# Kernel tuning notes

Measured on AMD Instinct MI355X. Metric: run time of the kernel, lower is better.

The kernel has to match this reference:

```python
import jax, jax.numpy as jnp
import numpy as np

B, N, C_IN = 8, 8192, 64
M, K, RADIUS = 1024, 64, 0.2
MLP = [64, 64, 128]


def _fps(pts, m):
    """Iterative farthest point sampling. pts: [N,3] -> [m] int32 indices."""
    n = pts.shape[0]

    def step(carry, _):
        dists, last = carry
        d = jnp.sum((pts - pts[last]) ** 2, axis=-1)          # [N]
        dists = jnp.minimum(dists, d)
        nxt = jnp.argmax(dists).astype(jnp.int32)
        return (dists, nxt), nxt

    init = (jnp.full((n,), 1e10, pts.dtype), jnp.int32(0))
    _, idx = jax.lax.scan(step, init, None, length=m - 1)
    return jnp.concatenate([jnp.zeros((1,), jnp.int32), idx])


def _ball_query(new_xyz, xyz, radius, k):
    """new_xyz: [B,3,M], xyz: [B,3,N] -> [B,M,K] neighbor indices.
    First k points within radius (in index order); padded with first hit."""
    d2 = (jnp.sum(new_xyz ** 2, 1)[:, :, None] + jnp.sum(xyz ** 2, 1)[:, None, :]
          - 2.0 * jnp.einsum('bcm,bcn->bmn', new_xyz, xyz))   # [B,M,N]
    mask = d2 < radius * radius
    # stable argsort of ~mask puts indices of in-radius points first, in order
    order = jnp.argsort(jnp.where(mask, 0, 1).astype(jnp.int32), axis=-1)[..., :k]
    count = jnp.sum(mask, axis=-1)                             # [B,M]
    valid = jnp.arange(k)[None, None, :] < count[..., None]
    return jnp.where(valid, order, order[..., :1])


def _group(x, idx):
    """x: [B,C,N], idx: [B,...] -> [B,C,...] gathered along N."""
    return jax.vmap(lambda a, i: a[:, i])(x, idx)


def _forward(xyz, feature, params):
    # FPS centroid indices (torch runs under no_grad -> stop_gradient)
    pts = jax.lax.stop_gradient(jnp.transpose(xyz, (0, 2, 1)))  # [B,N,3]
    cidx = jax.vmap(lambda p: _fps(p, M))(pts)                  # [B,M]
    new_xyz = _group(xyz, cidx)                                 # [B,3,M]
    nidx = _ball_query(jax.lax.stop_gradient(new_xyz),
                       jax.lax.stop_gradient(xyz), RADIUS, K)   # [B,M,K]
    gxyz = _group(xyz, nidx) - new_xyz[..., None]               # [B,3,M,K]
    x = jnp.concatenate([gxyz, _group(feature, nidx)], axis=1)  # [B,3+C,M,K]
    # SharedMLP: 1x1 conv2d + BN (folded to per-channel scale/bias) + ReLU
    for w, s, b in params:
        x = jax.nn.relu(jnp.einsum('oi,bimk->bomk', w, x)
                        * s[:, None, None] + b[:, None, None])
    return new_xyz, jnp.max(x, axis=3)                          # [B,3,M], [B,128,M]


def setup_inputs() -> dict:
    key = jax.random.key(0)
    ks = jax.random.split(key, 5)
    inp = {
        'xyz': jax.random.normal(ks[0], (B, 3, N), jnp.float32),
        'feature': jax.random.normal(ks[1], (B, C_IN, N), jnp.float32),
    }
    prev = C_IN + 3  # use_xyz=True
    for li, co in enumerate(MLP):
        inp[f'w{li}'] = jax.random.normal(ks[2 + li], (co, prev), jnp.float32) / np.sqrt(prev).astype(np.float32)
        inp[f's{li}'] = jnp.ones((co,), jnp.float32)
        inp[f'b{li}'] = jnp.zeros((co,), jnp.float32)
        prev = co
    return inp


def reference(xyz, feature, w0, s0, b0, w1, s1, b1, w2, s2, b2):
    return _forward(xyz, feature, ((w0, s0, b0), (w1, s1, b1), (w2, s2, b2)))
```

## Files before the change

### kernel.cpp

```cpp
#include <hip/hip_runtime.h>


#define B_ 8
#define N_ 8192
#define M_ 1024
#define K_ 64
#define FTW 68

typedef float vf2 __attribute__((ext_vector_type(2)));

template <int CTRL>
__device__ __forceinline__ unsigned long long dpp_key(unsigned long long k) {
  int lo = __builtin_amdgcn_update_dpp(0, (int)(unsigned int)k, CTRL, 0xF, 0xF, true);
  int hi = __builtin_amdgcn_update_dpp(0, (int)(unsigned int)(k >> 32), CTRL, 0xF, 0xF, true);
  unsigned long long o = ((unsigned long long)(unsigned int)hi << 32) | (unsigned int)lo;
  return o > k ? o : k;
}

__global__ __launch_bounds__(256) void fps_ft_kernel(const float* __restrict__ xyz,
                                                     const float* __restrict__ feat,
                                                     float* __restrict__ ft,
                                                     float* __restrict__ nxyz) {
#pragma clang fp contract(off)
  if (blockIdx.x >= 8) {
    const int nb = gridDim.x - 8;
    const int total = B_ * N_ * FTW;
    for (int idx = (blockIdx.x - 8) * 256 + threadIdx.x; idx < total; idx += nb * 256) {
      int c = idx % FTW;
      int bn = idx / FTW;
      int n = bn & (N_ - 1);
      int b = bn >> 13;
      float v;
      if (c < 3) v = xyz[(b * 3 + c) * N_ + n];
      else if (c < 67) v = feat[(b * 64 + (c - 3)) * N_ + n];
      else v = 0.f;
      ft[idx] = v;
    }
    return;
  }

  __shared__ float4 pts4[N_];
  __shared__ unsigned long long cand[2][16];
  __shared__ int scidx[M_];
  const int b = blockIdx.x;
  const int t = threadIdx.x;
  const int lane = t & 63;
  const int wid = t >> 6;
  const float* xb = xyz + b * 3 * N_;

  for (int n = t; n < N_; n += 256) {
    pts4[n] = make_float4(xb[n], xb[N_ + n], xb[2 * N_ + n], 0.f);
  }

  const int base = t * 32;
  const vf2* xv = (const vf2*)(xb + base);
  const vf2* yv = (const vf2*)(xb + N_ + base);
  const vf2* zv = (const vf2*)(xb + 2 * N_ + base);
  vf2 px2[16], py2[16], pz2[16], mind2[16];
#pragma unroll
  for (int j = 0; j < 16; ++j) {
    px2[j] = xv[j];
    py2[j] = yv[j];
    pz2[j] = zv[j];
    mind2[j] = vf2{1e10f, 1e10f};
  }
  float xl = xb[0], yl = xb[N_], zl = xb[2 * N_];
  if (t == 0) scidx[0] = 0;
  __syncthreads();

  for (int i = 1; i < M_; ++i) {
    const vf2 xl2 = vf2{xl, xl}, yl2 = vf2{yl, yl}, zl2 = vf2{zl, zl};
    float bestv = -1.f;
    int bl = 0;
#pragma unroll
    for (int j = 0; j < 16; ++j) {
      vf2 dx = px2[j] - xl2;
      vf2 dy = py2[j] - yl2;
      vf2 dz = pz2[j] - zl2;
      vf2 d = (dx * dx + dy * dy) + dz * dz;
      vf2 md;
      md.x = fminf(mind2[j].x, d.x);
      md.y = fminf(mind2[j].y, d.y);
      mind2[j] = md;
      if (md.x > bestv) { bestv = md.x; bl = 2 * j; }
      if (md.y > bestv) { bestv = md.y; bl = 2 * j + 1; }
    }
    unsigned long long key =
        ((unsigned long long)__float_as_uint(bestv) << 32) | (unsigned int)(~(base + bl));
    key = dpp_key<0xB1>(key);
    key = dpp_key<0x4E>(key);
    key = dpp_key<0x141>(key);
    key = dpp_key<0x140>(key);
    if ((lane & 15) == 0) cand[i & 1][wid * 4 + (lane >> 4)] = key;
    __syncthreads();
    unsigned long long gk = cand[i & 1][lane & 15];
    gk = dpp_key<0xB1>(gk);
    gk = dpp_key<0x4E>(gk);
    gk = dpp_key<0x141>(gk);
    gk = dpp_key<0x140>(gk);
    const int gi = (int)(~(unsigned int)gk);
    if (t == 0) scidx[i] = gi;
    float4 cc = pts4[gi];
    xl = cc.x; yl = cc.y; zl = cc.z;
  }
  __syncthreads();
  for (int q = t; q < M_; q += 256) {
    int ci = scidx[q];
    float4 c = pts4[ci];
    nxyz[b * 3 * M_ + q] = c.x;
    nxyz[b * 3 * M_ + M_ + q] = c.y;
    nxyz[b * 3 * M_ + 2 * M_ + q] = c.z;
  }
}

__global__ __launch_bounds__(256) void ballq_kernel(const float* __restrict__ xyz,
                                                    const float* __restrict__ nxyz,
                                                    int* __restrict__ nidx) {
  const int lane = threadIdx.x & 63;
  const int g = blockIdx.x * 4 + (threadIdx.x >> 6);
  const int b = g >> 10;
  const int m = g & (M_ - 1);
  const float* xb = xyz + b * 3 * N_;
  const float cx = nxyz[b * 3 * M_ + m];
  const float cy = nxyz[b * 3 * M_ + M_ + m];
  const float cz = nxyz[b * 3 * M_ + 2 * M_ + m];
  const float nc = __fadd_rn(__fadd_rn(__fmul_rn(cx, cx), __fmul_rn(cy, cy)), __fmul_rn(cz, cz));
  int cnt = 0;
  int first = 0;
  int* slot = nidx + (g << 6);
  for (int basei = 0; basei < N_ && cnt < K_; basei += 64) {
    const int n = basei + lane;
    float p_x = xb[n], p_y = xb[N_ + n], p_z = xb[2 * N_ + n];
    float pn = __fadd_rn(__fadd_rn(__fmul_rn(p_x, p_x), __fmul_rn(p_y, p_y)), __fmul_rn(p_z, p_z));
    float dt = __fadd_rn(__fadd_rn(__fmul_rn(cx, p_x), __fmul_rn(cy, p_y)), __fmul_rn(cz, p_z));
    float d2 = __fsub_rn(__fadd_rn(nc, pn), __fmul_rn(2.f, dt));
    bool inr = d2 < 0.04f;
    unsigned long long mk = __ballot(inr);
    if (cnt == 0 && mk != 0ull) first = basei + (__ffsll((long long)mk) - 1);
    int pos = cnt + (int)__popcll(mk & ((1ull << lane) - 1ull));
    if (inr && pos < K_) slot[pos] = n;
    cnt += (int)__popcll(mk);
  }
  if (cnt > K_) cnt = K_;
  if (lane >= cnt) slot[lane] = first;
}

template <bool USE_FT>
__global__ __launch_bounds__(64) void mlp_kernel(
    const float* __restrict__ ft, const float* __restrict__ xyz, const float* __restrict__ feat,
    const int* __restrict__ nidx, const float* __restrict__ nxyz,
    const float* __restrict__ w0, const float* __restrict__ s0, const float* __restrict__ b0,
    const float* __restrict__ w1, const float* __restrict__ s1, const float* __restrict__ b1,
    const float* __restrict__ w2, const float* __restrict__ s2, const float* __restrict__ b2,
    float* __restrict__ out2) {
  __shared__ float ylds[64 * 65];
  const int g = blockIdx.x;
  const int b = g >> 10;
  const int m = g & (M_ - 1);
  const int lane = threadIdx.x;
  const int n = nidx[(g << 6) + lane];
  const float cx = nxyz[b * 3 * M_ + m];
  const float cy = nxyz[b * 3 * M_ + M_ + m];
  const float cz = nxyz[b * 3 * M_ + 2 * M_ + m];

  float x0[67];
  if (USE_FT) {
    const float4* row = (const float4*)(ft + (size_t)((b << 13) + n) * FTW);
    float f[FTW];
#pragma unroll
    for (int q = 0; q < 17; ++q) {
      float4 v = row[q];
      f[q * 4 + 0] = v.x; f[q * 4 + 1] = v.y; f[q * 4 + 2] = v.z; f[q * 4 + 3] = v.w;
    }
    x0[0] = f[0] - cx; x0[1] = f[1] - cy; x0[2] = f[2] - cz;
#pragma unroll
    for (int c = 3; c < 67; ++c) x0[c] = f[c];
  } else {
    const float* xb = xyz + b * 3 * N_;
    x0[0] = xb[n] - cx; x0[1] = xb[N_ + n] - cy; x0[2] = xb[2 * N_ + n] - cz;
#pragma unroll
    for (int c = 0; c < 64; ++c) x0[3 + c] = feat[((b << 6) + c) * N_ + n];
  }

  for (int o = 0; o < 64; o += 4) {
    const float* wr = w0 + o * 67;
    float a0 = 0.f, a1 = 0.f, a2 = 0.f, a3 = 0.f;
#pragma unroll
    for (int ci = 0; ci < 67; ++ci) {
      float xvv = x0[ci];
      a0 = fmaf(wr[ci], xvv, a0);
      a1 = fmaf(wr[67 + ci], xvv, a1);
      a2 = fmaf(wr[134 + ci], xvv, a2);
      a3 = fmaf(wr[201 + ci], xvv, a3);
    }
    ylds[lane * 65 + o + 0] = fmaxf(fmaf(a0, s0[o + 0], b0[o + 0]), 0.f);
    ylds[lane * 65 + o + 1] = fmaxf(fmaf(a1, s0[o + 1], b0[o + 1]), 0.f);
    ylds[lane * 65 + o + 2] = fmaxf(fmaf(a2, s0[o + 2], b0[o + 2]), 0.f);
    ylds[lane * 65 + o + 3] = fmaxf(fmaf(a3, s0[o + 3], b0[o + 3]), 0.f);
  }
  float x1[64];
#pragma unroll
  for (int c = 0; c < 64; ++c) x1[c] = ylds[lane * 65 + c];

  for (int o = 0; o < 64; o += 4) {
    const float* wr = w1 + o * 64;
    float a0 = 0.f, a1 = 0.f, a2 = 0.f, a3 = 0.f;
#pragma unroll
    for (int ci = 0; ci < 64; ++ci) {
      float xvv = x1[ci];
      a0 = fmaf(wr[ci], xvv, a0);
      a1 = fmaf(wr[64 + ci], xvv, a1);
      a2 = fmaf(wr[128 + ci], xvv, a2);
      a3 = fmaf(wr[192 + ci], xvv, a3);
    }
    ylds[lane * 65 + o + 0] = fmaxf(fmaf(a0, s1[o + 0], b1[o + 0]), 0.f);
    ylds[lane * 65 + o + 1] = fmaxf(fmaf(a1, s1[o + 1], b1[o + 1]), 0.f);
    ylds[lane * 65 + o + 2] = fmaxf(fmaf(a2, s1[o + 2], b1[o + 2]), 0.f);
    ylds[lane * 65 + o + 3] = fmaxf(fmaf(a3, s1[o + 3], b1[o + 3]), 0.f);
  }
  float x2[64];
#pragma unroll
  for (int c = 0; c < 64; ++c) x2[c] = ylds[lane * 65 + c];

  float* outbm = out2 + (size_t)(b * 128) * M_ + m;
  for (int o = 0; o < 128; o += 4) {
    const float* wr = w2 + o * 64;
    float a0 = 0.f, a1 = 0.f, a2 = 0.f, a3 = 0.f;
#pragma unroll
    for (int ci = 0; ci < 64; ++ci) {
      float xvv = x2[ci];
      a0 = fmaf(wr[ci], xvv, a0);
      a1 = fmaf(wr[64 + ci], xvv, a1);
      a2 = fmaf(wr[128 + ci], xvv, a2);
      a3 = fmaf(wr[192 + ci], xvv, a3);
    }
    float v0 = fmaxf(fmaf(a0, s2[o + 0], b2[o + 0]), 0.f);
    float v1 = fmaxf(fmaf(a1, s2[o + 1], b2[o + 1]), 0.f);
    float v2 = fmaxf(fmaf(a2, s2[o + 2], b2[o + 2]), 0.f);
    float v3 = fmaxf(fmaf(a3, s2[o + 3], b2[o + 3]), 0.f);
#pragma unroll
    for (int off = 32; off > 0; off >>= 1) {
      v0 = fmaxf(v0, __shfl_xor(v0, off, 64));
      v1 = fmaxf(v1, __shfl_xor(v1, off, 64));
      v2 = fmaxf(v2, __shfl_xor(v2, off, 64));
      v3 = fmaxf(v3, __shfl_xor(v3, off, 64));
    }
    if (lane == ((o + 0) & 63)) outbm[(o + 0) * M_] = v0;
    if (lane == ((o + 1) & 63)) outbm[(o + 1) * M_] = v1;
    if (lane == ((o + 2) & 63)) outbm[(o + 2) * M_] = v2;
    if (lane == ((o + 3) & 63)) outbm[(o + 3) * M_] = v3;
  }
}

extern "C" void kernel_launch(void* const* d_in, const int* in_sizes, int n_in,
                              void* d_out, int out_size, void* d_ws, size_t ws_size,
                              hipStream_t stream) {
  const float* xyz = (const float*)d_in[0];
  const float* feat = (const float*)d_in[1];
  const float* w0 = (const float*)d_in[2];
  const float* s0 = (const float*)d_in[3];
  const float* b0 = (const float*)d_in[4];
  const float* w1 = (const float*)d_in[5];
  const float* s1 = (const float*)d_in[6];
  const float* b1 = (const float*)d_in[7];
  const float* w2 = (const float*)d_in[8];
  const float* s2 = (const float*)d_in[9];
  const float* b2 = (const float*)d_in[10];

  float* nxyz = (float*)d_out;
  float* out2 = (float*)d_out + B_ * 3 * M_;

  const size_t nidx_bytes = (size_t)B_ * M_ * K_ * sizeof(int);
  const size_t ft_bytes = (size_t)B_ * N_ * FTW * sizeof(float);
  int* nidx = (int*)d_ws;
  float* ft = (float*)((char*)d_ws + nidx_bytes);
  const bool use_ft = ws_size >= nidx_bytes + ft_bytes;

  hipLaunchKernelGGL(fps_ft_kernel, dim3(use_ft ? 64 : 8), dim3(256), 0, stream,
                     xyz, feat, ft, nxyz);
  hipLaunchKernelGGL(ballq_kernel, dim3(B_ * M_ / 4), dim3(256), 0, stream, xyz, nxyz, nidx);
  if (use_ft) {
    hipLaunchKernelGGL((mlp_kernel<true>), dim3(B_ * M_), dim3(64), 0, stream,
                       ft, xyz, feat, nidx, nxyz, w0, s0, b0, w1, s1, b1, w2, s2, b2, out2);
  } else {
    hipLaunchKernelGGL((mlp_kernel<false>), dim3(B_ * M_), dim3(64), 0, stream,
                       ft, xyz, feat, nidx, nxyz, w0, s0, b0, w1, s1, b1, w2, s2, b2, out2);
  }
}
```

Baseline: 1.398 ms.

## Split FPS argmax into float max reduction plus index recovery; use DPP max in MLP

The FPS loop no longer carries a packed 64-bit (value, index) key through the per-point compare and the DPP reduction. It now reduces only the float max with 32-bit DPP row/broadcast ops, picks the block max from four per-wave candidates, and then only the winning waves rescan their registers for the lowest matching index, combined with a wave umin and a shared atomicMin. The 64-bit key work per step shrinks, but a second __syncthreads and a rescan pass are added to every iteration. The MLP max reduction also swaps shuffle-xor for DPP plus readlane.

```diff
diff --git a/kernel.cpp b/kernel.cpp
--- a/kernel.cpp
+++ b/kernel.cpp
@@ -7,14 +7,34 @@
 #define K_ 64
 #define FTW 68
 
-typedef float vf2 __attribute__((ext_vector_type(2)));
-
 template <int CTRL>
-__device__ __forceinline__ unsigned long long dpp_key(unsigned long long k) {
-  int lo = __builtin_amdgcn_update_dpp(0, (int)(unsigned int)k, CTRL, 0xF, 0xF, true);
-  int hi = __builtin_amdgcn_update_dpp(0, (int)(unsigned int)(k >> 32), CTRL, 0xF, 0xF, true);
-  unsigned long long o = ((unsigned long long)(unsigned int)hi << 32) | (unsigned int)lo;
-  return o > k ? o : k;
+__device__ __forceinline__ float dpp_fmax(float v) {
+  int o = __builtin_amdgcn_update_dpp(0, __float_as_int(v), CTRL, 0xF, 0xF, true);
+  return fmaxf(v, __int_as_float(o));
+}
+__device__ __forceinline__ float wave_fmax63(float v) {
+  v = dpp_fmax<0xB1>(v);
+  v = dpp_fmax<0x4E>(v);
+  v = dpp_fmax<0x141>(v);
+  v = dpp_fmax<0x140>(v);
+  v = dpp_fmax<0x142>(v);
+  v = dpp_fmax<0x143>(v);
+  return v;
+}
+template <int CTRL>
+__device__ __forceinline__ unsigned int dpp_umin(unsigned int v) {
+  int o = __builtin_amdgcn_update_dpp(0, (int)v, CTRL, 0xF, 0xF, true);
+  unsigned int ov = (unsigned int)o;
+  return ov < v ? ov : v;
+}
+__device__ __forceinline__ unsigned int wave_umin63(unsigned int v) {
+  v = dpp_umin<0xB1>(v);
+  v = dpp_umin<0x4E>(v);
+  v = dpp_umin<0x141>(v);
+  v = dpp_umin<0x140>(v);
+  v = dpp_umin<0x142>(v);
+  v = dpp_umin<0x143>(v);
+  return v;
 }
 
 __global__ __launch_bounds__(256) void fps_ft_kernel(const float* __restrict__ xyz,
@@ -40,7 +60,8 @@
   }
 
   __shared__ float4 pts4[N_];
-  __shared__ unsigned long long cand[2][16];
+  __shared__ float candv[4];
+  __shared__ unsigned int sidx[2];
   __shared__ int scidx[M_];
   const int b = blockIdx.x;
   const int t = threadIdx.x;
@@ -53,63 +74,65 @@
   }
 
   const int base = t * 32;
-  const vf2* xv = (const vf2*)(xb + base);
-  const vf2* yv = (const vf2*)(xb + N_ + base);
-  const vf2* zv = (const vf2*)(xb + 2 * N_ + base);
-  vf2 px2[16], py2[16], pz2[16], mind2[16];
-#pragma unroll
-  for (int j = 0; j < 16; ++j) {
-    px2[j] = xv[j];
-    py2[j] = yv[j];
-    pz2[j] = zv[j];
-    mind2[j] = vf2{1e10f, 1e10f};
+  float px[32], py[32], pz[32], mind[32];
+#pragma unroll
+  for (int j = 0; j < 32; ++j) {
+    px[j] = xb[base + j];
+    py[j] = xb[N_ + base + j];
+    pz[j] = xb[2 * N_ + base + j];
+    mind[j] = 1e10f;
   }
   float xl = xb[0], yl = xb[N_], zl = xb[2 * N_];
-  if (t == 0) scidx[0] = 0;
+  if (t == 0) {
+    scidx[0] = 0;
+    sidx[0] = 0xFFFFFFFFu;
+    sidx[1] = 0xFFFFFFFFu;
+  }
   __syncthreads();
 
   for (int i = 1; i < M_; ++i) {
-    const vf2 xl2 = vf2{xl, xl}, yl2 = vf2{yl, yl}, zl2 = vf2{zl, zl};
+    const int q = i & 1;
     float bestv = -1.f;
-    int bl = 0;
-#pragma unroll
-    for (int j = 0; j < 16; ++j) {
-      vf2 dx = px2[j] - xl2;
-      vf2 dy = py2[j] - yl2;
-      vf2 dz = pz2[j] - zl2;
-      vf2 d = (dx * dx + dy * dy) + dz * dz;
-      vf2 md;
-      md.x = fminf(mind2[j].x, d.x);
-      md.y = fminf(mind2[j].y, d.y);
-      mind2[j] = md;
-      if (md.x > bestv) { bestv = md.x; bl = 2 * j; }
-      if (md.y > bestv) { bestv = md.y; bl = 2 * j + 1; }
-    }
-    unsigned long long key =
-        ((unsigned long long)__float_as_uint(bestv) << 32) | (unsigned int)(~(base + bl));
-    key = dpp_key<0xB1>(key);
-    key = dpp_key<0x4E>(key);
-    key = dpp_key<0x141>(key);
-    key = dpp_key<0x140>(key);
-    if ((lane & 15) == 0) cand[i & 1][wid * 4 + (lane >> 4)] = key;
+#pragma unroll
+    for (int j = 0; j < 32; ++j) {
+      float dx = __fsub_rn(px[j], xl);
+      float dy = __fsub_rn(py[j], yl);
+      float dz = __fsub_rn(pz[j], zl);
+      float d = __fadd_rn(__fadd_rn(__fmul_rn(dx, dx), __fmul_rn(dy, dy)), __fmul_rn(dz, dz));
+      float md = fminf(mind[j], d);
+      mind[j] = md;
+      bestv = fmaxf(bestv, md);
+    }
+    float wv = wave_fmax63(bestv);
+    const int wvbits = __builtin_amdgcn_readlane(__float_as_int(wv), 63);
+    if (lane == 63) candv[wid] = wv;
     __syncthreads();
-    unsigned long long gk = cand[i & 1][lane & 15];
-    gk = dpp_key<0xB1>(gk);
-    gk = dpp_key<0x4E>(gk);
-    gk = dpp_key<0x141>(gk);
-    gk = dpp_key<0x140>(gk);
-    const int gi = (int)(~(unsigned int)gk);
-    if (t == 0) scidx[i] = gi;
+    const float4 cv = *(const float4*)candv;
+    const float bmax = fmaxf(fmaxf(cv.x, cv.y), fmaxf(cv.z, cv.w));
+    const int bmaxbits = __builtin_amdgcn_readfirstlane(__float_as_int(bmax));
+    if (t == 0) sidx[1 - q] = 0xFFFFFFFFu;
+    if (wvbits == bmaxbits) {
+      int myj = 64;
+#pragma unroll
+      for (int j = 31; j >= 0; --j)
+        if (__float_as_int(mind[j]) == bmaxbits) myj = j;
+      unsigned int myidx = (myj < 64) ? (unsigned int)(base + myj) : 0xFFFFFFFFu;
+      unsigned int mi = wave_umin63(myidx);
+      if (lane == 63) atomicMin(&sidx[q], mi);
+    }
+    __syncthreads();
+    const unsigned int gi = sidx[q];
+    if (t == 0) scidx[i] = (int)gi;
     float4 cc = pts4[gi];
     xl = cc.x; yl = cc.y; zl = cc.z;
   }
   __syncthreads();
-  for (int q = t; q < M_; q += 256) {
-    int ci = scidx[q];
+  for (int qi = t; qi < M_; qi += 256) {
+    int ci = scidx[qi];
     float4 c = pts4[ci];
-    nxyz[b * 3 * M_ + q] = c.x;
-    nxyz[b * 3 * M_ + M_ + q] = c.y;
-    nxyz[b * 3 * M_ + 2 * M_ + q] = c.z;
+    nxyz[b * 3 * M_ + qi] = c.x;
+    nxyz[b * 3 * M_ + M_ + qi] = c.y;
+    nxyz[b * 3 * M_ + 2 * M_ + qi] = c.z;
   }
 }
 
@@ -238,17 +261,18 @@
     float v1 = fmaxf(fmaf(a1, s2[o + 1], b2[o + 1]), 0.f);
     float v2 = fmaxf(fmaf(a2, s2[o + 2], b2[o + 2]), 0.f);
     float v3 = fmaxf(fmaf(a3, s2[o + 3], b2[o + 3]), 0.f);
-#pragma unroll
-    for (int off = 32; off > 0; off >>= 1) {
-      v0 = fmaxf(v0, __shfl_xor(v0, off, 64));
-      v1 = fmaxf(v1, __shfl_xor(v1, off, 64));
-      v2 = fmaxf(v2, __shfl_xor(v2, off, 64));
-      v3 = fmaxf(v3, __shfl_xor(v3, off, 64));
-    }
-    if (lane == ((o + 0) & 63)) outbm[(o + 0) * M_] = v0;
-    if (lane == ((o + 1) & 63)) outbm[(o + 1) * M_] = v1;
-    if (lane == ((o + 2) & 63)) outbm[(o + 2) * M_] = v2;
-    if (lane == ((o + 3) & 63)) outbm[(o + 3) * M_] = v3;
+    v0 = wave_fmax63(v0);
+    v1 = wave_fmax63(v1);
+    v2 = wave_fmax63(v2);
+    v3 = wave_fmax63(v3);
+    float g0 = __int_as_float(__builtin_amdgcn_readlane(__float_as_int(v0), 63));
+    float g1 = __int_as_float(__builtin_amdgcn_readlane(__float_as_int(v1), 63));
+    float g2 = __int_as_float(__builtin_amdgcn_readlane(__float_as_int(v2), 63));
+    float g3 = __int_as_float(__builtin_amdgcn_readlane(__float_as_int(v3), 63));
+    if (lane == ((o + 0) & 63)) outbm[(o + 0) * M_] = g0;
+    if (lane == ((o + 1) & 63)) outbm[(o + 1) * M_] = g1;
+    if (lane == ((o + 2) & 63)) outbm[(o + 2) * M_] = g2;
+    if (lane == ((o + 3) & 63)) outbm[(o + 3) * M_] = g3;
   }
 }
 
```

After: 1.579 ms. 12.9% more time.
